# Kernel tuning notes

Measured on AMD Instinct MI355X. Metric: run time of the kernel, lower is better.

## Reference

```python
import jax, jax.numpy as jnp
import numpy as np

B, D, NQ, NS = 64, 64, 2048, 2048

def setup_inputs() -> dict:
    key = jax.random.key(0)
    k1, k2 = jax.random.split(key)
    query_local = jax.random.normal(k1, (B, D, NQ), dtype=jnp.float32)
    support_local = jax.random.normal(k2, (B, D, NS), dtype=jnp.float32)
    return {"query_local": query_local, "support_local": support_local}

def reference(query_local, support_local):
    # sim[b, q, s] = sum_d query[b, d, q] * support[b, d, s]  -> (B, N_q, N_s)
    sim = jnp.einsum('bdq,bds->bqs', query_local, support_local)
    best_sim = jnp.max(sim, axis=2)        # (B, N_q)
    return jnp.mean(best_sim, axis=1)      # (B,)
```

## Files before the change

### kernel.cpp

```cpp
#include <hip/hip_runtime.h>
#include <hip/hip_bf16.h>

#define NB 64
#define ND 64
#define NQ 2048
#define NS 2048
#define QBLK 256
#define SBLK 64
#define QPB 8

typedef float f32x4 __attribute__((ext_vector_type(4)));
typedef short bf16x8 __attribute__((ext_vector_type(8)));
typedef int i32x4 __attribute__((ext_vector_type(4)));

__device__ inline unsigned short f2bf(float v) {
  union { float f; unsigned u; } x; x.f = v;
  unsigned r = x.u + 0x7fffu + ((x.u >> 16) & 1u);
  return (unsigned short)(r >> 16);
}

__global__ __launch_bounds__(256, 2) void bmd_main(
    const float* __restrict__ Q, const float* __restrict__ S,
    float* __restrict__ part) {
  const int bid = blockIdx.x;
  const int b  = bid & (NB - 1);
  const int qb = bid >> 6;
  const int q0 = qb * QBLK;
  const int tid = threadIdx.x;
  const int lane = tid & 63;
  const int w = tid >> 6;

  __shared__ i32x4 sT4[SBLK * 8];
  __shared__ float wsum[4];
  char* sT = (char*)sT4;

  const float* Qb = Q + (size_t)b * ND * NQ;
  const float* Sb = S + (size_t)b * ND * NS;

  bf16x8 afrag[4][2];
  {
    const int qrow = q0 + w * 64 + (lane & 15);
    const int dbase = (lane >> 4) * 8;
    for (int mf = 0; mf < 4; ++mf)
      for (int ks = 0; ks < 2; ++ks) {
        const int d0 = ks * 32 + dbase;
        bf16x8 f;
        #pragma unroll
        for (int e = 0; e < 8; ++e)
          f[e] = (short)f2bf(Qb[(size_t)(d0 + e) * NQ + (qrow + mf * 16)]);
        afrag[mf][ks] = f;
      }
  }

  f32x4 rmax[4];
  for (int mf = 0; mf < 4; ++mf)
    rmax[mf] = f32x4{-INFINITY, -INFINITY, -INFINITY, -INFINITY};

  const int dbq = (tid >> 3) & 7;
  const int sl0 = (tid & 7) + ((tid >> 6) << 3);

  for (int s0 = 0; s0 < NS; s0 += SBLK) {
    __syncthreads();
    #pragma unroll
    for (int i = 0; i < 2; ++i) {
      const int sl = sl0 + i * 32;
      const float* src = Sb + (size_t)dbq * 8 * NS + (s0 + sl);
      bf16x8 pk;
      #pragma unroll
      for (int e = 0; e < 8; ++e) pk[e] = (short)f2bf(src[(size_t)e * NS]);
      const int byt = sl * 128 + ((dbq ^ (sl & 7)) << 4);
      *reinterpret_cast<bf16x8*>(sT + byt) = pk;
    }
    __syncthreads();

    #pragma unroll
    for (int nf = 0; nf < 4; ++nf) {
      const int scol = nf * 16 + (lane & 15);
      bf16x8 bfr[2];
      #pragma unroll
      for (int ks = 0; ks < 2; ++ks) {
        const int slot = (ks * 4 + (lane >> 4)) ^ (scol & 7);
        bfr[ks] = *reinterpret_cast<const bf16x8*>(sT + scol * 128 + (slot << 4));
      }
      #pragma unroll
      for (int mf = 0; mf < 4; ++mf) {
        f32x4 acc = {0.f, 0.f, 0.f, 0.f};
        acc = __builtin_amdgcn_mfma_f32_16x16x32_bf16(afrag[mf][0], bfr[0], acc, 0, 0, 0);
        acc = __builtin_amdgcn_mfma_f32_16x16x32_bf16(afrag[mf][1], bfr[1], acc, 0, 0, 0);
        #pragma unroll
        for (int j = 0; j < 4; ++j) rmax[mf][j] = fmaxf(rmax[mf][j], acc[j]);
      }
    }
  }

  float qsum = 0.f;
  for (int mf = 0; mf < 4; ++mf)
    for (int j = 0; j < 4; ++j) {
      float v = rmax[mf][j];
      v = fmaxf(v, __shfl_xor(v, 1));
      v = fmaxf(v, __shfl_xor(v, 2));
      v = fmaxf(v, __shfl_xor(v, 4));
      v = fmaxf(v, __shfl_xor(v, 8));
      qsum += v;
    }
  qsum += __shfl_xor(qsum, 16);
  qsum += __shfl_xor(qsum, 32);
  if (lane == 0) wsum[w] = qsum;
  __syncthreads();
  if (tid == 0)
    part[b * QPB + qb] = wsum[0] + wsum[1] + wsum[2] + wsum[3];
}

__global__ void bmd_reduce(const float* __restrict__ part, float* __restrict__ out) {
  const int b = threadIdx.x;
  float s = 0.f;
  for (int i = 0; i < QPB; ++i) s += part[b * QPB + i];
  out[b] = s * (1.0f / NQ);
}

extern "C" void kernel_launch(void* const* d_in, const int* in_sizes, int n_in,
                              void* d_out, int out_size, void* d_ws, size_t ws_size,
                              hipStream_t stream) {
  const float* Q = (const float*)d_in[0];
  const float* S = (const float*)d_in[1];
  float* out = (float*)d_out;
  float* part = (float*)d_ws;
  bmd_main<<<dim3(NB * QPB), dim3(256), 0, stream>>>(Q, S, part);
  bmd_reduce<<<dim3(1), dim3(NB), 0, stream>>>(part, out);
}
```

Measured before the change: 46.67 us.

## Split support dimension across blocks and double-buffer support tiles in LDS

Doubles the grid by splitting the support axis into two halves, so each block computes per-query row maxima over half of S. These are written per row to the workspace, and a rewritten reduce kernel takes the max across halves before averaging. The S staging loop is also double-buffered: the next tile's global loads are issued before the MFMA work on the current tile and converted into the alternate LDS buffer afterwards. Launch bounds are raised to 4 blocks per CU. The intent is better CU occupancy (512 blocks previously on 256 CUs) and hiding global load latency. The cost is more workspace traffic, a heavier reduce, and more register pressure from the prefetch buffers.

Result: no change. 45.84 us (-1.8%).

```diff
diff --git a/kernel.cpp b/kernel.cpp
--- a/kernel.cpp
+++ b/kernel.cpp
@@ -1,5 +1,4 @@
 #include <hip/hip_runtime.h>
-#include <hip/hip_bf16.h>
 
 #define NB 64
 #define ND 64
@@ -8,10 +7,12 @@
 #define QBLK 256
 #define SBLK 64
 #define QPB 8
+#define NSPLIT 2
+#define NSS (NS / NSPLIT)
+#define NT (NSS / SBLK)
 
 typedef float f32x4 __attribute__((ext_vector_type(4)));
 typedef short bf16x8 __attribute__((ext_vector_type(8)));
-typedef int i32x4 __attribute__((ext_vector_type(4)));
 
 __device__ inline unsigned short f2bf(float v) {
   union { float f; unsigned u; } x; x.f = v;
@@ -19,20 +20,20 @@
   return (unsigned short)(r >> 16);
 }
 
-__global__ __launch_bounds__(256, 2) void bmd_main(
+__global__ __launch_bounds__(256, 4) void bmd_main(
     const float* __restrict__ Q, const float* __restrict__ S,
     float* __restrict__ part) {
   const int bid = blockIdx.x;
   const int b  = bid & (NB - 1);
-  const int qb = bid >> 6;
+  const int qb = (bid >> 6) & (QPB - 1);
+  const int ss = bid >> 9;
   const int q0 = qb * QBLK;
+  const int sbase = ss * NSS;
   const int tid = threadIdx.x;
   const int lane = tid & 63;
   const int w = tid >> 6;
 
-  __shared__ i32x4 sT4[SBLK * 8];
-  __shared__ float wsum[4];
-  char* sT = (char*)sT4;
+  __shared__ char sT[2][SBLK * 128];
 
   const float* Qb = Q + (size_t)b * ND * NQ;
   const float* Sb = S + (size_t)b * ND * NS;
@@ -53,25 +54,42 @@
   }
 
   f32x4 rmax[4];
+  #pragma unroll
   for (int mf = 0; mf < 4; ++mf)
     rmax[mf] = f32x4{-INFINITY, -INFINITY, -INFINITY, -INFINITY};
 
   const int dbq = (tid >> 3) & 7;
-  const int sl0 = (tid & 7) + ((tid >> 6) << 3);
+  const int sl0 = (tid & 7) + (w << 3);
+  const float* stage_src = Sb + (size_t)dbq * 8 * NS + sbase;
+  int sl[2], byt[2];
+  #pragma unroll
+  for (int i = 0; i < 2; ++i) {
+    sl[i] = sl0 + i * 32;
+    byt[i] = sl[i] * 128 + ((dbq ^ (sl[i] & 7)) << 4);
+  }
 
-  for (int s0 = 0; s0 < NS; s0 += SBLK) {
-    __syncthreads();
+  #pragma unroll
+  for (int i = 0; i < 2; ++i) {
+    const float* src = stage_src + sl[i];
+    bf16x8 pk;
     #pragma unroll
-    for (int i = 0; i < 2; ++i) {
-      const int sl = sl0 + i * 32;
-      const float* src = Sb + (size_t)dbq * 8 * NS + (s0 + sl);
-      bf16x8 pk;
+    for (int e = 0; e < 8; ++e) pk[e] = (short)f2bf(src[(size_t)e * NS]);
+    *reinterpret_cast<bf16x8*>(sT[0] + byt[i]) = pk;
+  }
+  __syncthreads();
+
+  int cur = 0;
+  for (int t = 0; t < NT; ++t) {
+    float pf[2][8];
+    const bool has_next = (t + 1 < NT);
+    if (has_next) {
+      const float* src = stage_src + (t + 1) * SBLK;
       #pragma unroll
-      for (int e = 0; e < 8; ++e) pk[e] = (short)f2bf(src[(size_t)e * NS]);
-      const int byt = sl * 128 + ((dbq ^ (sl & 7)) << 4);
-      *reinterpret_cast<bf16x8*>(sT + byt) = pk;
+      for (int i = 0; i < 2; ++i)
+        #pragma unroll
+        for (int e = 0; e < 8; ++e)
+          pf[i][e] = src[sl[i] + (size_t)e * NS];
     }
-    __syncthreads();
 
     #pragma unroll
     for (int nf = 0; nf < 4; ++nf) {
@@ -80,7 +98,7 @@
       #pragma unroll
       for (int ks = 0; ks < 2; ++ks) {
         const int slot = (ks * 4 + (lane >> 4)) ^ (scol & 7);
-        bfr[ks] = *reinterpret_cast<const bf16x8*>(sT + scol * 128 + (slot << 4));
+        bfr[ks] = *reinterpret_cast<const bf16x8*>(sT[cur] + scol * 128 + (slot << 4));
       }
       #pragma unroll
       for (int mf = 0; mf < 4; ++mf) {
@@ -91,31 +109,51 @@
         for (int j = 0; j < 4; ++j) rmax[mf][j] = fmaxf(rmax[mf][j], acc[j]);
       }
     }
+
+    if (has_next) {
+      #pragma unroll
+      for (int i = 0; i < 2; ++i) {
+        bf16x8 pk;
+        #pragma unroll
+        for (int e = 0; e < 8; ++e) pk[e] = (short)f2bf(pf[i][e]);
+        *reinterpret_cast<bf16x8*>(sT[cur ^ 1] + byt[i]) = pk;
+      }
+    }
+    __syncthreads();
+    cur ^= 1;
   }
 
-  float qsum = 0.f;
-  for (int mf = 0; mf < 4; ++mf)
+  float* rowp = part + (size_t)bid * QBLK + w * 64;
+  #pragma unroll
+  for (int mf = 0; mf < 4; ++mf) {
+    #pragma unroll
     for (int j = 0; j < 4; ++j) {
       float v = rmax[mf][j];
       v = fmaxf(v, __shfl_xor(v, 1));
       v = fmaxf(v, __shfl_xor(v, 2));
       v = fmaxf(v, __shfl_xor(v, 4));
       v = fmaxf(v, __shfl_xor(v, 8));
-      qsum += v;
+      if ((lane & 15) == 0)
+        rowp[mf * 16 + (lane >> 4) * 4 + j] = v;
     }
-  qsum += __shfl_xor(qsum, 16);
-  qsum += __shfl_xor(qsum, 32);
-  if (lane == 0) wsum[w] = qsum;
-  __syncthreads();
-  if (tid == 0)
-    part[b * QPB + qb] = wsum[0] + wsum[1] + wsum[2] + wsum[3];
+  }
 }
 
 __global__ void bmd_reduce(const float* __restrict__ part, float* __restrict__ out) {
-  const int b = threadIdx.x;
-  float s = 0.f;
-  for (int i = 0; i < QPB; ++i) s += part[b * QPB + i];
-  out[b] = s * (1.0f / NQ);
+  const int b = blockIdx.x;
+  const int tid = threadIdx.x;
+  __shared__ float ws4[4];
+  float sum = 0.f;
+  for (int qb = 0; qb < QPB; ++qb) {
+    const float v0 = part[((size_t)(qb * NB + b)) * QBLK + tid];
+    const float v1 = part[((size_t)(NB * QPB + qb * NB + b)) * QBLK + tid];
+    sum += fmaxf(v0, v1);
+  }
+  #pragma unroll
+  for (int o = 1; o < 64; o <<= 1) sum += __shfl_xor(sum, o);
+  if ((tid & 63) == 0) ws4[tid >> 6] = sum;
+  __syncthreads();
+  if (tid == 0) out[b] = (ws4[0] + ws4[1] + ws4[2] + ws4[3]) * (1.0f / NQ);
 }
 
 extern "C" void kernel_launch(void* const* d_in, const int* in_sizes, int n_in,
@@ -125,6 +163,6 @@
   const float* S = (const float*)d_in[1];
   float* out = (float*)d_out;
   float* part = (float*)d_ws;
-  bmd_main<<<dim3(NB * QPB), dim3(256), 0, stream>>>(Q, S, part);
-  bmd_reduce<<<dim3(1), dim3(NB), 0, stream>>>(part, out);
+  bmd_main<<<dim3(NB * QPB * NSPLIT), dim3(256), 0, stream>>>(Q, S, part);
+  bmd_reduce<<<dim3(NB), dim3(256), 0, stream>>>(part, out);
 }
```
